# Kernel tuning notes

Hardware: AMD Instinct MI355X
Metric: run time of the kernel (lower is better)

## Reference

```python
import jax, jax.numpy as jnp
import numpy as np

N_SPEAKERS, N_UTTER, EMB_DIM = 1024, 20, 256


def setup_inputs() -> dict:
    key = jax.random.key(0)
    k_in, = jax.random.split(key, 1)
    inp = jax.random.normal(k_in, (N_SPEAKERS, N_UTTER, EMB_DIM), dtype=jnp.float32)
    w = jnp.asarray(10.0, dtype=jnp.float32)
    b = jnp.asarray(-5.0, dtype=jnp.float32)
    return {"input": inp, "w": w, "b": b}


def reference(input, w, b):
    # input: [N, M, D] utterance embeddings
    N, M, D = input.shape
    centroids = jnp.mean(input, axis=1)                       # [N, D]
    # leave-one-out centroid for each (speaker, utterance):
    # mean of the other M-1 utterances of the same speaker
    excl = (centroids[:, None, :] * M - input) / (M - 1)      # [N, M, D]

    inv_u = 1.0 / jnp.linalg.norm(input, axis=-1, keepdims=True)      # [N, M, 1]
    u_hat = input * inv_u                                             # [N, M, D]
    c_hat = centroids / jnp.linalg.norm(centroids, axis=-1, keepdims=True)  # [N, D]
    e_hat = excl / jnp.linalg.norm(excl, axis=-1, keepdims=True)      # [N, M, D]

    # cosine sim of every utterance vs every full centroid
    cs = jnp.einsum('nmd,kd->nmk', u_hat, c_hat)              # [N, M, N]
    # override k == own speaker with the excluded-centroid cosine
    cs_self = jnp.sum(u_hat * e_hat, axis=-1)                 # [N, M]
    idx = jnp.arange(N)
    cs = cs.at[idx, :, idx].set(cs_self)

    sim = w * cs + b                                          # scaled similarity
    logp = jax.nn.log_softmax(sim, axis=-1)                   # softmax over speakers
    loss = -jnp.sum(logp[idx, :, idx])
    return loss
```

## Files before the change

### kernel.cpp

```cpp
#include <hip/hip_runtime.h>
#include <hip/hip_fp8.h>


#define D_DIM 256
#define N_SPK 1024
#define M_UTT 20

typedef long lx2 __attribute__((ext_vector_type(2)));
typedef float f32x16 __attribute__((ext_vector_type(16)));

__device__ __forceinline__ int pk4_fp8(float x0, float x1, float x2, float x3) {
#if __has_builtin(__builtin_amdgcn_cvt_pk_fp8_f32)
  int v = __builtin_amdgcn_cvt_pk_fp8_f32(x0, x1, 0, false);
  v = __builtin_amdgcn_cvt_pk_fp8_f32(x2, x3, v, true);
  return v;
#else
  union { int i; unsigned char b[4]; } u;
  u.b[0] = __hip_fp8_e4m3(x0).__x;
  u.b[1] = __hip_fp8_e4m3(x1).__x;
  u.b[2] = __hip_fp8_e4m3(x2).__x;
  u.b[3] = __hip_fp8_e4m3(x3).__x;
  return u.i;
#endif
}

__global__ __launch_bounds__(256) void ge2e_prep(
    const float* __restrict__ inp, unsigned int* __restrict__ bsw32,
    float* __restrict__ c_raw, float* __restrict__ ccv,
    float* __restrict__ out) {
  const int tid = threadIdx.x, lane = tid & 63, wv = tid >> 6;
  const int s = blockIdx.x * 4 + wv;
  if (blockIdx.x == 0 && tid == 0) out[0] = 0.0f;

  const float4* up =
      reinterpret_cast<const float4*>(inp + (size_t)s * (M_UTT * D_DIM)) + lane;
  float4 a = make_float4(0.f, 0.f, 0.f, 0.f);
#pragma unroll
  for (int m = 0; m < M_UTT; ++m) {
    const float4 f = up[m * (D_DIM / 4)];
    a.x += f.x; a.y += f.y; a.z += f.z; a.w += f.w;
  }
  const float inv = 1.0f / (float)M_UTT;
  const float4 c = make_float4(a.x * inv, a.y * inv, a.z * inv, a.w * inv);
  reinterpret_cast<float4*>(c_raw + (size_t)s * D_DIM)[lane] = c;

  float cc = c.x * c.x + c.y * c.y + c.z * c.z + c.w * c.w;
#pragma unroll
  for (int o = 1; o < 64; o <<= 1) cc += __shfl_xor(cc, o, 64);
  if (lane == 0) ccv[s] = cc;

  const float r = rsqrtf(fmaxf(cc, 1e-20f));
  const int q = pk4_fp8(c.x * r, c.y * r, c.z * r, c.w * r);
  const int t = s >> 5, n5 = s & 31;
  const int p = lane >> 3, sub = (lane >> 2) & 1;
  const int half = (lane >> 1) & 1, jb = (lane & 1) * 4;
  bsw32[((((t * 8 + p) * 64) + half * 32 + n5) * 16 + sub * 8 + jb) >> 2] =
      (unsigned int)q;
}

__global__ __launch_bounds__(256, 2) void ge2e_main(
    const float* __restrict__ inp, const float* __restrict__ wp,
    const unsigned char* __restrict__ bsw, const float* __restrict__ c_raw,
    const float* __restrict__ ccv, float* __restrict__ out) {
  __shared__ __align__(16) unsigned char lA[32 * D_DIM];
  __shared__ float uuL[32], ucL[32], ccL[32];
  __shared__ float rowtot[4][32];
  const int tid = threadIdx.x;
  const int r0 = blockIdx.x * 32;
  const float w = wp[0];

  {
    const int m = tid >> 3, seg = tid & 7;
    const int r = r0 + m, nr = r / M_UTT;
    const float4* urow =
        reinterpret_cast<const float4*>(inp + (size_t)r * D_DIM + seg * 32);
    const float4* crow =
        reinterpret_cast<const float4*>(c_raw + (size_t)nr * D_DIM + seg * 32);
    float4 uf[8];
    float uu = 0.f, uc = 0.f;
#pragma unroll
    for (int q = 0; q < 8; ++q) {
      uf[q] = urow[q];
      const float4 cf = crow[q];
      uu += uf[q].x * uf[q].x + uf[q].y * uf[q].y + uf[q].z * uf[q].z +
            uf[q].w * uf[q].w;
      uc += uf[q].x * cf.x + uf[q].y * cf.y + uf[q].z * cf.z + uf[q].w * cf.w;
    }
#pragma unroll
    for (int o = 1; o < 8; o <<= 1) {
      uu += __shfl_xor(uu, o, 64);
      uc += __shfl_xor(uc, o, 64);
    }
    const float s = w * rsqrtf(fmaxf(uu, 1e-20f));
    int4 ch0, ch1;
    ch0.x = pk4_fp8(s * uf[0].x, s * uf[0].y, s * uf[0].z, s * uf[0].w);
    ch0.y = pk4_fp8(s * uf[1].x, s * uf[1].y, s * uf[1].z, s * uf[1].w);
    ch0.z = pk4_fp8(s * uf[4].x, s * uf[4].y, s * uf[4].z, s * uf[4].w);
    ch0.w = pk4_fp8(s * uf[5].x, s * uf[5].y, s * uf[5].z, s * uf[5].w);
    ch1.x = pk4_fp8(s * uf[2].x, s * uf[2].y, s * uf[2].z, s * uf[2].w);
    ch1.y = pk4_fp8(s * uf[3].x, s * uf[3].y, s * uf[3].z, s * uf[3].w);
    ch1.z = pk4_fp8(s * uf[6].x, s * uf[6].y, s * uf[6].z, s * uf[6].w);
    ch1.w = pk4_fp8(s * uf[7].x, s * uf[7].y, s * uf[7].z, s * uf[7].w);
    reinterpret_cast<int4*>(lA)[seg * 64 + m] = ch0;
    reinterpret_cast<int4*>(lA)[seg * 64 + m + 32] = ch1;
    if (seg == 0) {
      uuL[m] = uu;
      ucL[m] = uc;
      ccL[m] = ccv[nr];
    }
  }
  __syncthreads();

  const int lane = tid & 63, wv = tid >> 6, hl = lane >> 5;
  lx2 A[8];
  const lx2* lAv = reinterpret_cast<const lx2*>(lA);
#pragma unroll
  for (int p = 0; p < 8; ++p) A[p] = lAv[p * 64 + lane];

  float sume[16];
#pragma unroll
  for (int i = 0; i < 16; ++i) sume[i] = 0.0f;

  const lx2* Bbase =
      reinterpret_cast<const lx2*>(bsw) + (size_t)(wv * 8) * 512 + lane;
  lx2 Bc[8];
#pragma unroll
  for (int p = 0; p < 8; ++p) Bc[p] = Bbase[p * 64];
#pragma unroll
  for (int t = 0; t < 8; ++t) {
    lx2 Bn[8];
    if (t < 7) {
      const lx2* Bt = Bbase + (t + 1) * 512;
#pragma unroll
      for (int p = 0; p < 8; ++p) Bn[p] = Bt[p * 64];
    }
    f32x16 acc0, acc1;
#pragma unroll
    for (int i = 0; i < 16; ++i) { acc0[i] = 0.0f; acc1[i] = 0.0f; }
#pragma unroll
    for (int p = 0; p < 8; ++p) {
      acc0 = __builtin_amdgcn_mfma_f32_32x32x16_fp8_fp8(A[p].x, Bc[p].x, acc0,
                                                        0, 0, 0);
      acc1 = __builtin_amdgcn_mfma_f32_32x32x16_fp8_fp8(A[p].y, Bc[p].y, acc1,
                                                        0, 0, 0);
    }
#pragma unroll
    for (int i = 0; i < 16; ++i)
      sume[i] += __expf(fminf(acc0[i] + acc1[i], 40.0f));
    if (t < 7) {
#pragma unroll
      for (int p = 0; p < 8; ++p) Bc[p] = Bn[p];
    }
  }

#pragma unroll
  for (int i = 0; i < 16; ++i) {
    float v = sume[i];
#pragma unroll
    for (int o = 1; o < 32; o <<= 1) v += __shfl_xor(v, o, 64);
    sume[i] = v;
  }
  if ((lane & 31) == 0) {
#pragma unroll
    for (int i = 0; i < 16; ++i)
      rowtot[wv][(i & 3) + 8 * (i >> 2) + 4 * hl] = sume[i];
  }
  __syncthreads();

  if (tid < 32) {
    const float se0 = rowtot[0][tid] + rowtot[1][tid] + rowtot[2][tid] +
                      rowtot[3][tid];
    const float uu = uuL[tid], uc = ucL[tid], cc = ccL[tid];
    const float Mf = (float)M_UTT;
    const float ue = (Mf * uc - uu) * (1.0f / (Mf - 1.0f));
    const float ee = (Mf * Mf * cc - 2.0f * Mf * uc + uu) *
                     (1.0f / ((Mf - 1.0f) * (Mf - 1.0f)));
    const float sself = w * ue * rsqrtf(fmaxf(uu * ee, 1e-20f));
    const float sown = w * uc * rsqrtf(fmaxf(uu * cc, 1e-20f));
    const float se = fmaxf(
        se0 + __expf(fminf(sself, 40.f)) - __expf(fminf(sown, 40.f)), 1e-10f);
    float v = __logf(se) - sself;
#pragma unroll
    for (int o = 1; o < 32; o <<= 1) v += __shfl_xor(v, o, 64);
    if (tid == 0) atomicAdd(out, v);
  }
}

extern "C" void kernel_launch(void* const* d_in, const int* in_sizes, int n_in,
                              void* d_out, int out_size, void* d_ws, size_t ws_size,
                              hipStream_t stream) {
  const float* inp = (const float*)d_in[0];
  const float* wp  = (const float*)d_in[1];
  float* out = (float*)d_out;

  unsigned char* bsw = (unsigned char*)d_ws;
  float* c_raw = (float*)((char*)d_ws + 256 * 1024);
  float* ccv   = c_raw + (size_t)N_SPK * D_DIM;

  ge2e_prep<<<N_SPK / 4, 256, 0, stream>>>(inp, (unsigned int*)bsw, c_raw, ccv,
                                           out);
  ge2e_main<<<(N_SPK * M_UTT) / 32, 256, 0, stream>>>(inp, wp, bsw, c_raw, ccv,
                                                      out);
}
```

Before: 92.34 us.

## Process 64 utterance rows per block to halve centroid matrix reloads

```diff
diff --git a/kernel.cpp b/kernel.cpp
--- a/kernel.cpp
+++ b/kernel.cpp
@@ -5,6 +5,7 @@
 #define D_DIM 256
 #define N_SPK 1024
 #define M_UTT 20
+#define ROWS  64
 
 typedef long lx2 __attribute__((ext_vector_type(2)));
 typedef float f32x16 __attribute__((ext_vector_type(16)));
@@ -62,24 +63,24 @@
     const float* __restrict__ inp, const float* __restrict__ wp,
     const unsigned char* __restrict__ bsw, const float* __restrict__ c_raw,
     const float* __restrict__ ccv, float* __restrict__ out) {
-  __shared__ __align__(16) unsigned char lA[32 * D_DIM];
-  __shared__ float uuL[32], ucL[32], ccL[32];
-  __shared__ float rowtot[4][32];
+  __shared__ __align__(16) unsigned char lA[ROWS * D_DIM];
+  __shared__ float uuL[ROWS], ucL[ROWS], ccL[ROWS];
+  __shared__ float rowtot[4][ROWS];
   const int tid = threadIdx.x;
-  const int r0 = blockIdx.x * 32;
+  const int r0 = blockIdx.x * ROWS;
   const float w = wp[0];
 
   {
-    const int m = tid >> 3, seg = tid & 7;
+    const int m = tid >> 2, seg = tid & 3;
     const int r = r0 + m, nr = r / M_UTT;
     const float4* urow =
-        reinterpret_cast<const float4*>(inp + (size_t)r * D_DIM + seg * 32);
+        reinterpret_cast<const float4*>(inp + (size_t)r * D_DIM + seg * 64);
     const float4* crow =
-        reinterpret_cast<const float4*>(c_raw + (size_t)nr * D_DIM + seg * 32);
-    float4 uf[8];
+        reinterpret_cast<const float4*>(c_raw + (size_t)nr * D_DIM + seg * 64);
+    float4 uf[16];
     float uu = 0.f, uc = 0.f;
 #pragma unroll
-    for (int q = 0; q < 8; ++q) {
+    for (int q = 0; q < 16; ++q) {
       uf[q] = urow[q];
       const float4 cf = crow[q];
       uu += uf[q].x * uf[q].x + uf[q].y * uf[q].y + uf[q].z * uf[q].z +
@@ -87,22 +88,29 @@
       uc += uf[q].x * cf.x + uf[q].y * cf.y + uf[q].z * cf.z + uf[q].w * cf.w;
     }
 #pragma unroll
-    for (int o = 1; o < 8; o <<= 1) {
+    for (int o = 1; o < 4; o <<= 1) {
       uu += __shfl_xor(uu, o, 64);
       uc += __shfl_xor(uc, o, 64);
     }
     const float s = w * rsqrtf(fmaxf(uu, 1e-20f));
-    int4 ch0, ch1;
-    ch0.x = pk4_fp8(s * uf[0].x, s * uf[0].y, s * uf[0].z, s * uf[0].w);
-    ch0.y = pk4_fp8(s * uf[1].x, s * uf[1].y, s * uf[1].z, s * uf[1].w);
-    ch0.z = pk4_fp8(s * uf[4].x, s * uf[4].y, s * uf[4].z, s * uf[4].w);
-    ch0.w = pk4_fp8(s * uf[5].x, s * uf[5].y, s * uf[5].z, s * uf[5].w);
-    ch1.x = pk4_fp8(s * uf[2].x, s * uf[2].y, s * uf[2].z, s * uf[2].w);
-    ch1.y = pk4_fp8(s * uf[3].x, s * uf[3].y, s * uf[3].z, s * uf[3].w);
-    ch1.z = pk4_fp8(s * uf[6].x, s * uf[6].y, s * uf[6].z, s * uf[6].w);
-    ch1.w = pk4_fp8(s * uf[7].x, s * uf[7].y, s * uf[7].z, s * uf[7].w);
-    reinterpret_cast<int4*>(lA)[seg * 64 + m] = ch0;
-    reinterpret_cast<int4*>(lA)[seg * 64 + m + 32] = ch1;
+    const int H = m >> 5, m31 = m & 31;
+    int4* dst = reinterpret_cast<int4*>(lA) + H * 512 + m31;
+#pragma unroll
+    for (int pp = 0; pp < 2; ++pp) {
+      const int p = 2 * seg + pp;
+      const float4* f = uf + pp * 8;
+      int4 ch0, ch1;
+      ch0.x = pk4_fp8(s * f[0].x, s * f[0].y, s * f[0].z, s * f[0].w);
+      ch0.y = pk4_fp8(s * f[1].x, s * f[1].y, s * f[1].z, s * f[1].w);
+      ch0.z = pk4_fp8(s * f[4].x, s * f[4].y, s * f[4].z, s * f[4].w);
+      ch0.w = pk4_fp8(s * f[5].x, s * f[5].y, s * f[5].z, s * f[5].w);
+      ch1.x = pk4_fp8(s * f[2].x, s * f[2].y, s * f[2].z, s * f[2].w);
+      ch1.y = pk4_fp8(s * f[3].x, s * f[3].y, s * f[3].z, s * f[3].w);
+      ch1.z = pk4_fp8(s * f[6].x, s * f[6].y, s * f[6].z, s * f[6].w);
+      ch1.w = pk4_fp8(s * f[7].x, s * f[7].y, s * f[7].z, s * f[7].w);
+      dst[p * 64] = ch0;
+      dst[p * 64 + 32] = ch1;
+    }
     if (seg == 0) {
       uuL[m] = uu;
       ucL[m] = uc;
@@ -112,62 +120,69 @@
   __syncthreads();
 
   const int lane = tid & 63, wv = tid >> 6, hl = lane >> 5;
-  lx2 A[8];
   const lx2* lAv = reinterpret_cast<const lx2*>(lA);
-#pragma unroll
-  for (int p = 0; p < 8; ++p) A[p] = lAv[p * 64 + lane];
-
-  float sume[16];
-#pragma unroll
-  for (int i = 0; i < 16; ++i) sume[i] = 0.0f;
-
-  const lx2* Bbase =
-      reinterpret_cast<const lx2*>(bsw) + (size_t)(wv * 8) * 512 + lane;
-  lx2 Bc[8];
-#pragma unroll
-  for (int p = 0; p < 8; ++p) Bc[p] = Bbase[p * 64];
-#pragma unroll
+  lx2 A0[8], A1[8];
+#pragma unroll
+  for (int p = 0; p < 8; ++p) {
+    A0[p] = lAv[p * 64 + lane];
+    A1[p] = lAv[512 + p * 64 + lane];
+  }
+
+  float sume0[16], sume1[16];
+#pragma unroll
+  for (int i = 0; i < 16; ++i) { sume0[i] = 0.0f; sume1[i] = 0.0f; }
+
+  const lx2* Bv = reinterpret_cast<const lx2*>(bsw);
+#pragma unroll 1
   for (int t = 0; t < 8; ++t) {
-    lx2 Bn[8];
-    if (t < 7) {
-      const lx2* Bt = Bbase + (t + 1) * 512;
-#pragma unroll
-      for (int p = 0; p < 8; ++p) Bn[p] = Bt[p * 64];
-    }
-    f32x16 acc0, acc1;
-#pragma unroll
-    for (int i = 0; i < 16; ++i) { acc0[i] = 0.0f; acc1[i] = 0.0f; }
+    const lx2* Bt = Bv + (size_t)(wv * 8 + t) * 512 + lane;
+    lx2 B[8];
+#pragma unroll
+    for (int p = 0; p < 8; ++p) B[p] = Bt[p * 64];
+    f32x16 a00, a01, a10, a11;
+#pragma unroll
+    for (int i = 0; i < 16; ++i) {
+      a00[i] = 0.0f; a01[i] = 0.0f; a10[i] = 0.0f; a11[i] = 0.0f;
+    }
 #pragma unroll
     for (int p = 0; p < 8; ++p) {
-      acc0 = __builtin_amdgcn_mfma_f32_32x32x16_fp8_fp8(A[p].x, Bc[p].x, acc0,
-                                                        0, 0, 0);
-      acc1 = __builtin_amdgcn_mfma_f32_32x32x16_fp8_fp8(A[p].y, Bc[p].y, acc1,
-                                                        0, 0, 0);
-    }
-#pragma unroll
-    for (int i = 0; i < 16; ++i)
-      sume[i] += __expf(fminf(acc0[i] + acc1[i], 40.0f));
-    if (t < 7) {
-#pragma unroll
-      for (int p = 0; p < 8; ++p) Bc[p] = Bn[p];
+      a00 = __builtin_amdgcn_mfma_f32_32x32x16_fp8_fp8(A0[p].x, B[p].x, a00,
+                                                       0, 0, 0);
+      a01 = __builtin_amdgcn_mfma_f32_32x32x16_fp8_fp8(A0[p].y, B[p].y, a01,
+                                                       0, 0, 0);
+      a10 = __builtin_amdgcn_mfma_f32_32x32x16_fp8_fp8(A1[p].x, B[p].x, a10,
+                                                       0, 0, 0);
+      a11 = __builtin_amdgcn_mfma_f32_32x32x16_fp8_fp8(A1[p].y, B[p].y, a11,
+                                                       0, 0, 0);
+    }
+#pragma unroll
+    for (int i = 0; i < 16; ++i) {
+      sume0[i] += __expf(fminf(a00[i] + a01[i], 40.0f));
+      sume1[i] += __expf(fminf(a10[i] + a11[i], 40.0f));
     }
   }
 
 #pragma unroll
   for (int i = 0; i < 16; ++i) {
-    float v = sume[i];
-#pragma unroll
-    for (int o = 1; o < 32; o <<= 1) v += __shfl_xor(v, o, 64);
-    sume[i] = v;
+    float v0 = sume0[i], v1 = sume1[i];
+#pragma unroll
+    for (int o = 1; o < 32; o <<= 1) {
+      v0 += __shfl_xor(v0, o, 64);
+      v1 += __shfl_xor(v1, o, 64);
+    }
+    sume0[i] = v0; sume1[i] = v1;
   }
   if ((lane & 31) == 0) {
 #pragma unroll
-    for (int i = 0; i < 16; ++i)
-      rowtot[wv][(i & 3) + 8 * (i >> 2) + 4 * hl] = sume[i];
+    for (int i = 0; i < 16; ++i) {
+      const int idx = (i & 3) + 8 * (i >> 2) + 4 * hl;
+      rowtot[wv][idx] = sume0[i];
+      rowtot[wv][32 + idx] = sume1[i];
+    }
   }
   __syncthreads();
 
-  if (tid < 32) {
+  if (tid < ROWS) {
     const float se0 = rowtot[0][tid] + rowtot[1][tid] + rowtot[2][tid] +
                       rowtot[3][tid];
     const float uu = uuL[tid], uc = ucL[tid], cc = ccL[tid];
@@ -181,7 +196,7 @@
         se0 + __expf(fminf(sself, 40.f)) - __expf(fminf(sown, 40.f)), 1e-10f);
     float v = __logf(se) - sself;
 #pragma unroll
-    for (int o = 1; o < 32; o <<= 1) v += __shfl_xor(v, o, 64);
+    for (int o = 1; o < 64; o <<= 1) v += __shfl_xor(v, o, 64);
     if (tid == 0) atomicAdd(out, v);
   }
 }
@@ -199,6 +214,6 @@
 
   ge2e_prep<<<N_SPK / 4, 256, 0, stream>>>(inp, (unsigned int*)bsw, c_raw, ccv,
                                            out);
-  ge2e_main<<<(N_SPK * M_UTT) / 32, 256, 0, stream>>>(inp, wp, bsw, c_raw, ccv,
-                                                      out);
-}
+  ge2e_main<<<(N_SPK * M_UTT) / ROWS, 256, 0, stream>>>(inp, wp, bsw, c_raw,
+                                                        ccv, out);
+}
```

Result: slower. 94.37 us (+2.2%).
